# Kernel tuning notes

Measured on AMD Instinct MI355X. Metric: run time of the kernel, lower is better.

The kernel has to match this reference:

```python
import jax, jax.numpy as jnp
import numpy as np

B, T, D = 8192, 12, 512


def setup_inputs() -> dict:
    key = jax.random.key(0)
    ks = jax.random.split(key, 14)
    s = 1.0 / np.sqrt(D)
    return {
        "memory": jax.random.normal(ks[0], (B, D), jnp.float32),
        "info": jax.random.normal(ks[1], (B, D), jnp.float32),
        "control": jax.random.normal(ks[2], (B, D), jnp.float32),
        "contControl": jax.random.normal(ks[3], (B, D), jnp.float32),
        "allControls": jax.random.normal(ks[4], (B, T, D), jnp.float32),
        "allMemories": jax.random.normal(ks[5], (B, T, D), jnp.float32),
        # params (torch nn.Linear convention: W is [out, in])
        "Wc": jax.random.uniform(ks[6], (D, D), jnp.float32, -s, s),
        "bc": jax.random.uniform(ks[7], (D,), jnp.float32, -s, s),
        "Wa": jax.random.uniform(ks[8], (1, D), jnp.float32, -s, s),
        "ba": jax.random.uniform(ks[9], (1,), jnp.float32, -s, s),
        "Wl": jax.random.uniform(ks[10], (D, 3 * D), jnp.float32, -s, s),
        "bl": jax.random.uniform(ks[11], (D,), jnp.float32, -s, s),
        "Wg": jax.random.uniform(ks[12], (D, D), jnp.float32, -s, s),
        "bg": jax.random.uniform(ks[13], (D,), jnp.float32, -s, s),
    }


def reference(memory, info, control, contControl, allControls, allMemories,
              Wc, bc, Wa, ba, Wl, bl, Wg, bg):
    # self-attention over past memories (writeSelfAttMod == 'CONT')
    selfControl = contControl @ Wc.T + bc                      # [B, D]
    interactions = allControls * selfControl[:, None, :]       # [B, T, D]
    attn_logits = jnp.einsum("btd,od->bto", interactions, Wa)[..., 0] + ba[0]  # [B, T]
    attn = jax.nn.softmax(attn_logits, axis=1)                 # [B, T]
    selfSmry = jnp.einsum("bt,btd->bd", attn, allMemories)     # [B, D]
    # gated linear write
    newMemory = jnp.concatenate([memory, info, selfSmry], axis=-1) @ Wl.T + bl  # [B, D]
    z = jax.nn.sigmoid(control @ Wg.T + bg)                    # [B, D]
    return newMemory * z + memory * (1.0 - z)
```

## Files before the change

### kernel.cpp

```cpp
#include <hip/hip_runtime.h>
#include <stdint.h>
#include <math.h>


#define NB 8192
#define NT 12
#define ND 512

typedef short  bf16x8 __attribute__((ext_vector_type(8)));
typedef float  f32x4  __attribute__((ext_vector_type(4)));

__device__ __forceinline__ unsigned short f2bf(float x) {
    uint32_t u = __float_as_uint(x);
    uint32_t r = u + 0x7FFFu + ((u >> 16) & 1u);
    return (unsigned short)(r >> 16);
}
__device__ __forceinline__ float bf2f(unsigned short h) {
    return __uint_as_float(((uint32_t)h) << 16);
}

__global__ __launch_bounds__(256)
void wconv_kernel(const float* __restrict__ W, short* __restrict__ H,
                  short* __restrict__ L, int n4)
{
    int i = blockIdx.x * blockDim.x + threadIdx.x;
    if (i >= n4) return;
    float4 v = reinterpret_cast<const float4*>(W)[i];
    float xs[4] = {v.x, v.y, v.z, v.w};
    short4 hv, lv;
    short hh[4], ll[4];
#pragma unroll
    for (int j = 0; j < 4; ++j) {
        unsigned short h = f2bf(xs[j]);
        unsigned short l = f2bf(xs[j] - bf2f(h));
        hh[j] = (short)h; ll[j] = (short)l;
    }
    hv.x = hh[0]; hv.y = hh[1]; hv.z = hh[2]; hv.w = hh[3];
    lv.x = ll[0]; lv.y = ll[1]; lv.z = ll[2]; lv.w = ll[3];
    reinterpret_cast<short4*>(H)[i] = hv;
    reinterpret_cast<short4*>(L)[i] = lv;
}


template<bool AF32>
__device__ __forceinline__ void run_seg(
    const float* __restrict__ Af,
    const short* __restrict__ Aph, const short* __restrict__ Apl,
    const short* __restrict__ Wph, const short* __restrict__ Wpl,
    int sW,
    short* __restrict__ AhT, short* __restrict__ AlT,
    short* __restrict__ WhT, short* __restrict__ WlT,
    f32x4 (&acc)[4][2],
    const int soff, const int sr, const int sk,
    const int abase, const int wbase)
{
    float4 fa0, fa1;
    bf16x8 pah, pal, pwh, pwl;

    auto do_load = [&](int kt) {
        const int k = kt * 32 + sk;
        if constexpr (AF32) {
            fa0 = *reinterpret_cast<const float4*>(Af + (size_t)sr * ND + k);
            fa1 = *reinterpret_cast<const float4*>(Af + (size_t)sr * ND + k + 4);
        } else {
            pah = *reinterpret_cast<const bf16x8*>(Aph + (size_t)sr * ND + k);
            pal = *reinterpret_cast<const bf16x8*>(Apl + (size_t)sr * ND + k);
        }
        pwh = *reinterpret_cast<const bf16x8*>(Wph + (size_t)sr * sW + k);
        pwl = *reinterpret_cast<const bf16x8*>(Wpl + (size_t)sr * sW + k);
    };
    auto do_write = [&](int buf) {
        const int o = buf * 4096 + soff;
        if constexpr (AF32) {
            float xs[8] = {fa0.x, fa0.y, fa0.z, fa0.w, fa1.x, fa1.y, fa1.z, fa1.w};
            bf16x8 hv, lv;
#pragma unroll
            for (int j = 0; j < 8; ++j) {
                unsigned short h = f2bf(xs[j]);
                unsigned short l = f2bf(xs[j] - bf2f(h));
                hv[j] = (short)h; lv[j] = (short)l;
            }
            *reinterpret_cast<bf16x8*>(AhT + o) = hv;
            *reinterpret_cast<bf16x8*>(AlT + o) = lv;
        } else {
            *reinterpret_cast<bf16x8*>(AhT + o) = pah;
            *reinterpret_cast<bf16x8*>(AlT + o) = pal;
        }
        *reinterpret_cast<bf16x8*>(WhT + o) = pwh;
        *reinterpret_cast<bf16x8*>(WlT + o) = pwl;
    };

    do_load(0);
    do_write(0);
    __syncthreads();
    int cur = 0;
    for (int kt = 0; kt < 16; ++kt) {
        const bool pf = (kt + 1 < 16);
        if (pf) do_load(kt + 1);
        const int cb = cur * 4096;
        bf16x8 ah[4], al[4], wh[2], wl[2];
#pragma unroll
        for (int i = 0; i < 4; ++i) {
            ah[i] = *reinterpret_cast<const bf16x8*>(AhT + cb + abase + i * 512);
            al[i] = *reinterpret_cast<const bf16x8*>(AlT + cb + abase + i * 512);
        }
#pragma unroll
        for (int j = 0; j < 2; ++j) {
            wh[j] = *reinterpret_cast<const bf16x8*>(WhT + cb + wbase + j * 512);
            wl[j] = *reinterpret_cast<const bf16x8*>(WlT + cb + wbase + j * 512);
        }
#pragma unroll
        for (int i = 0; i < 4; ++i)
#pragma unroll
            for (int j = 0; j < 2; ++j) {
                acc[i][j] = __builtin_amdgcn_mfma_f32_16x16x32_bf16(ah[i], wh[j], acc[i][j], 0, 0, 0);
                acc[i][j] = __builtin_amdgcn_mfma_f32_16x16x32_bf16(ah[i], wl[j], acc[i][j], 0, 0, 0);
                acc[i][j] = __builtin_amdgcn_mfma_f32_16x16x32_bf16(al[i], wh[j], acc[i][j], 0, 0, 0);
            }
        if (pf) do_write(cur ^ 1);
        __syncthreads();
        cur ^= 1;
    }
}

#define GEMM_SETUP                                                         \
    const int t = threadIdx.x;                                             \
    const int bm = blockIdx.x, bn = blockIdx.y;                            \
    const int sr = t >> 2, scn = t & 3, sk = scn * 8;                      \
    const int soff = sr * 32 + (scn ^ ((sr >> 1) & 3)) * 8;                \
    const int w = t >> 6, wr = w >> 2, wc = w & 3;                         \
    const int lane = t & 63, fr = lane & 15, q = lane >> 4;                \
    const int rq = (q ^ ((fr >> 1) & 3)) * 8;                              \
    const int abase = (wr * 64 + fr) * 32 + rq;                            \
    const int wbase = (wc * 32 + fr) * 32 + rq;

__global__ __launch_bounds__(512, 2)
void gemm_selfcontrol(const float* __restrict__ cc,
                      const short* __restrict__ wch, const short* __restrict__ wcl,
                      const float* __restrict__ bc,
                      float* __restrict__ sc_out)
{
    __shared__ __align__(16) short AhT[2 * 4096], AlT[2 * 4096];
    __shared__ __align__(16) short WhT[2 * 4096], WlT[2 * 4096];
    GEMM_SETUP
    f32x4 acc[4][2];
    const f32x4 zz = {0.f, 0.f, 0.f, 0.f};
#pragma unroll
    for (int i = 0; i < 4; ++i) { acc[i][0] = zz; acc[i][1] = zz; }

    run_seg<true>(cc + (size_t)bm * 128 * ND, nullptr, nullptr,
                  wch + (size_t)(bn * 128) * ND, wcl + (size_t)(bn * 128) * ND, ND,
                  AhT, AlT, WhT, WlT, acc, soff, sr, sk, abase, wbase);

    const int c0 = bn * 128 + wc * 32 + fr;
    const float bc0 = bc[c0], bc1 = bc[c0 + 16];
#pragma unroll
    for (int i = 0; i < 4; ++i) {
        const int r = bm * 128 + wr * 64 + i * 16 + q * 4;
#pragma unroll
        for (int ri = 0; ri < 4; ++ri) {
            sc_out[(size_t)(r + ri) * ND + c0]      = acc[i][0][ri] + bc0;
            sc_out[(size_t)(r + ri) * ND + c0 + 16] = acc[i][1][ri] + bc1;
        }
    }
}

__global__ __launch_bounds__(512, 2)
void gemm_write(const float* __restrict__ memory, const float* __restrict__ info,
                const float* __restrict__ ctrl,
                const short* __restrict__ sh, const short* __restrict__ sl,
                const short* __restrict__ wlh, const short* __restrict__ wll,
                const short* __restrict__ wgh, const short* __restrict__ wgl,
                const float* __restrict__ bl_, const float* __restrict__ bg_,
                float* __restrict__ out)
{
    __shared__ __align__(16) short AhT[2 * 4096], AlT[2 * 4096];
    __shared__ __align__(16) short WhT[2 * 4096], WlT[2 * 4096];
    GEMM_SETUP
    f32x4 accN[4][2], accZ[4][2];
    const f32x4 zz = {0.f, 0.f, 0.f, 0.f};
#pragma unroll
    for (int i = 0; i < 4; ++i) {
        accN[i][0] = zz; accN[i][1] = zz;
        accZ[i][0] = zz; accZ[i][1] = zz;
    }

    const size_t ar = (size_t)bm * 128 * ND;
    const short* wlh_b = wlh + (size_t)(bn * 128) * 1536;
    const short* wll_b = wll + (size_t)(bn * 128) * 1536;

    run_seg<true >(memory + ar, nullptr, nullptr, wlh_b,        wll_b,        1536,
                   AhT, AlT, WhT, WlT, accN, soff, sr, sk, abase, wbase);
    run_seg<true >(info + ar,   nullptr, nullptr, wlh_b + 512,  wll_b + 512,  1536,
                   AhT, AlT, WhT, WlT, accN, soff, sr, sk, abase, wbase);
    run_seg<false>(nullptr, sh + ar, sl + ar,     wlh_b + 1024, wll_b + 1024, 1536,
                   AhT, AlT, WhT, WlT, accN, soff, sr, sk, abase, wbase);
    run_seg<true >(ctrl + ar,   nullptr, nullptr,
                   wgh + (size_t)(bn * 128) * ND, wgl + (size_t)(bn * 128) * ND, ND,
                   AhT, AlT, WhT, WlT, accZ, soff, sr, sk, abase, wbase);

    const int c0 = bn * 128 + wc * 32 + fr;
    const float blv[2] = {bl_[c0], bl_[c0 + 16]};
    const float bgv[2] = {bg_[c0], bg_[c0 + 16]};
#pragma unroll
    for (int i = 0; i < 4; ++i) {
        const int r = bm * 128 + wr * 64 + i * 16 + q * 4;
#pragma unroll
        for (int ri = 0; ri < 4; ++ri) {
#pragma unroll
            for (int j = 0; j < 2; ++j) {
                const int col = c0 + j * 16;
                const size_t idx = (size_t)(r + ri) * ND + col;
                const float nm = accN[i][j][ri] + blv[j];
                const float zl = accZ[i][j][ri] + bgv[j];
                const float z  = 1.f / (1.f + expf(-zl));
                const float m  = memory[idx];
                out[idx] = (nm - m) * z + m;
            }
        }
    }
}

__global__ __launch_bounds__(256)
void attn_kernel(const float* __restrict__ allControls,
                 const float* __restrict__ allMemories,
                 const float* __restrict__ selfControl,
                 const float* __restrict__ Wa,
                 const float* __restrict__ ba,
                 short* __restrict__ sh, short* __restrict__ sl)
{
    __shared__ float red[4][NT];
    __shared__ float lg[NT];
    const int b = blockIdx.x;
    const int t = threadIdx.x;
    const int lane = t & 63, wv = t >> 6;

    const float2 sc = ((const float2*)(selfControl + (size_t)b * ND))[t];
    const float2 wa = ((const float2*)Wa)[t];
    const float swx = sc.x * wa.x, swy = sc.y * wa.y;

    const float2* ac2 = (const float2*)(allControls + (size_t)b * NT * ND);
    float part[NT];
#pragma unroll
    for (int tt = 0; tt < NT; ++tt) {
        float2 v = ac2[tt * 256 + t];
        part[tt] = fmaf(v.x, swx, v.y * swy);
    }
#pragma unroll
    for (int tt = 0; tt < NT; ++tt) {
        float v = part[tt];
#pragma unroll
        for (int m = 1; m < 64; m <<= 1) v += __shfl_xor(v, m, 64);
        if (lane == 0) red[wv][tt] = v;
    }
    __syncthreads();
    if (t < NT) lg[t] = red[0][t] + red[1][t] + red[2][t] + red[3][t] + ba[0];
    __syncthreads();

    float l[NT], mx = -1e30f;
#pragma unroll
    for (int tt = 0; tt < NT; ++tt) { l[tt] = lg[tt]; mx = fmaxf(mx, l[tt]); }
    float e[NT], s = 0.f;
#pragma unroll
    for (int tt = 0; tt < NT; ++tt) { e[tt] = expf(l[tt] - mx); s += e[tt]; }
    const float inv = 1.f / s;

    const float2* am2 = (const float2*)(allMemories + (size_t)b * NT * ND);
    float ax = 0.f, ay = 0.f;
#pragma unroll
    for (int tt = 0; tt < NT; ++tt) {
        float2 v = am2[tt * 256 + t];
        const float wgt = e[tt] * inv;
        ax = fmaf(wgt, v.x, ax);
        ay = fmaf(wgt, v.y, ay);
    }
    unsigned short hx = f2bf(ax); unsigned short lx = f2bf(ax - bf2f(hx));
    unsigned short hy = f2bf(ay); unsigned short ly = f2bf(ay - bf2f(hy));
    short2 hv; hv.x = (short)hx; hv.y = (short)hy;
    short2 lv; lv.x = (short)lx; lv.y = (short)ly;
    reinterpret_cast<short2*>(sh + (size_t)b * ND)[t] = hv;
    reinterpret_cast<short2*>(sl + (size_t)b * ND)[t] = lv;
}

extern "C" void kernel_launch(void* const* d_in, const int* in_sizes, int n_in,
                              void* d_out, int out_size, void* d_ws, size_t ws_size,
                              hipStream_t stream) {
    const float* memory      = (const float*)d_in[0];
    const float* info        = (const float*)d_in[1];
    const float* control     = (const float*)d_in[2];
    const float* contControl = (const float*)d_in[3];
    const float* allControls = (const float*)d_in[4];
    const float* allMemories = (const float*)d_in[5];
    const float* Wc          = (const float*)d_in[6];
    const float* bc          = (const float*)d_in[7];
    const float* Wl          = (const float*)d_in[10];
    const float* bl          = (const float*)d_in[11];
    const float* Wg          = (const float*)d_in[12];
    const float* bg          = (const float*)d_in[13];
    float* out = (float*)d_out;

    char* wsb = (char*)d_ws;
    float* selfControl = (float*)wsb;
    short* sh  = (short*)(wsb + (size_t)16 * 1024 * 1024);
    short* sl  = sh  + (size_t)NB * ND;
    short* wch = sl  + (size_t)NB * ND;
    short* wcl = wch + 512 * 512;
    short* wlh = wcl + 512 * 512;
    short* wll = wlh + 512 * 1536;
    short* wgh = wll + 512 * 1536;
    short* wgl = wgh + 512 * 512;

    wconv_kernel<<<(512 * 512 / 4 + 255) / 256, 256, 0, stream>>>(Wc, wch, wcl, 512 * 512 / 4);
    wconv_kernel<<<(512 * 1536 / 4 + 255) / 256, 256, 0, stream>>>(Wl, wlh, wll, 512 * 1536 / 4);
    wconv_kernel<<<(512 * 512 / 4 + 255) / 256, 256, 0, stream>>>(Wg, wgh, wgl, 512 * 512 / 4);

    dim3 ggrid(NB / 128, ND / 128);
    gemm_selfcontrol<<<ggrid, 512, 0, stream>>>(contControl, wch, wcl,
                                                (const float*)d_in[7], selfControl);
    attn_kernel<<<NB, 256, 0, stream>>>(allControls, allMemories, selfControl,
                                        (const float*)d_in[8], (const float*)d_in[9],
                                        sh, sl);
    gemm_write<<<ggrid, 512, 0, stream>>>(memory, info, control, sh, sl,
                                          wlh, wll, wgh, wgl, bl, bg, out);
}
```

Measured before the change: 565.0 us.

## Use one wavefront per batch row in attention and merge weight conversions

The attention kernel now gives each batch row to a single 64-lane wavefront with 8 elements per lane. This removes the shared-memory reduction and both block barriers, and uses 16-byte vector loads and stores. The Wa scaling moves into the selfControl GEMM epilogue, so the attention kernel reads one precomputed vector. The bias ba is dropped because softmax does not change under a constant shift. The three weight-conversion launches are merged into one kernel to cut launch overhead.

```diff
diff --git a/kernel.cpp b/kernel.cpp
--- a/kernel.cpp
+++ b/kernel.cpp
@@ -20,25 +20,31 @@
 }
 
 __global__ __launch_bounds__(256)
-void wconv_kernel(const float* __restrict__ W, short* __restrict__ H,
-                  short* __restrict__ L, int n4)
-{
-    int i = blockIdx.x * blockDim.x + threadIdx.x;
-    if (i >= n4) return;
-    float4 v = reinterpret_cast<const float4*>(W)[i];
+void wconv_all(const float* __restrict__ Wc, const float* __restrict__ Wl,
+               const float* __restrict__ Wg,
+               short* __restrict__ wch, short* __restrict__ wcl,
+               short* __restrict__ wlh, short* __restrict__ wll,
+               short* __restrict__ wgh, short* __restrict__ wgl)
+{
+    int i = blockIdx.x * 256 + threadIdx.x;
+    const float* src; short* H; short* L; int j;
+    if (i < 65536)        { src = Wc; H = wch; L = wcl; j = i; }
+    else if (i < 262144)  { src = Wl; H = wlh; L = wll; j = i - 65536; }
+    else                  { src = Wg; H = wgh; L = wgl; j = i - 262144; }
+    float4 v = reinterpret_cast<const float4*>(src)[j];
     float xs[4] = {v.x, v.y, v.z, v.w};
     short4 hv, lv;
     short hh[4], ll[4];
 #pragma unroll
-    for (int j = 0; j < 4; ++j) {
-        unsigned short h = f2bf(xs[j]);
-        unsigned short l = f2bf(xs[j] - bf2f(h));
-        hh[j] = (short)h; ll[j] = (short)l;
+    for (int k = 0; k < 4; ++k) {
+        unsigned short h = f2bf(xs[k]);
+        unsigned short l = f2bf(xs[k] - bf2f(h));
+        hh[k] = (short)h; ll[k] = (short)l;
     }
     hv.x = hh[0]; hv.y = hh[1]; hv.z = hh[2]; hv.w = hh[3];
     lv.x = ll[0]; lv.y = ll[1]; lv.z = ll[2]; lv.w = ll[3];
-    reinterpret_cast<short4*>(H)[i] = hv;
-    reinterpret_cast<short4*>(L)[i] = lv;
+    reinterpret_cast<short4*>(H)[j] = hv;
+    reinterpret_cast<short4*>(L)[j] = lv;
 }
 
 
@@ -137,8 +143,8 @@
 __global__ __launch_bounds__(512, 2)
 void gemm_selfcontrol(const float* __restrict__ cc,
                       const short* __restrict__ wch, const short* __restrict__ wcl,
-                      const float* __restrict__ bc,
-                      float* __restrict__ sc_out)
+                      const float* __restrict__ bc, const float* __restrict__ Wa,
+                      float* __restrict__ v_out)
 {
     __shared__ __align__(16) short AhT[2 * 4096], AlT[2 * 4096];
     __shared__ __align__(16) short WhT[2 * 4096], WlT[2 * 4096];
@@ -154,13 +160,14 @@
 
     const int c0 = bn * 128 + wc * 32 + fr;
     const float bc0 = bc[c0], bc1 = bc[c0 + 16];
+    const float wa0 = Wa[c0], wa1 = Wa[c0 + 16];
 #pragma unroll
     for (int i = 0; i < 4; ++i) {
         const int r = bm * 128 + wr * 64 + i * 16 + q * 4;
 #pragma unroll
         for (int ri = 0; ri < 4; ++ri) {
-            sc_out[(size_t)(r + ri) * ND + c0]      = acc[i][0][ri] + bc0;
-            sc_out[(size_t)(r + ri) * ND + c0 + 16] = acc[i][1][ri] + bc1;
+            v_out[(size_t)(r + ri) * ND + c0]      = (acc[i][0][ri] + bc0) * wa0;
+            v_out[(size_t)(r + ri) * ND + c0 + 16] = (acc[i][1][ri] + bc1) * wa1;
         }
     }
 }
@@ -222,64 +229,67 @@
 }
 
 __global__ __launch_bounds__(256)
-void attn_kernel(const float* __restrict__ allControls,
-                 const float* __restrict__ allMemories,
-                 const float* __restrict__ selfControl,
-                 const float* __restrict__ Wa,
-                 const float* __restrict__ ba,
-                 short* __restrict__ sh, short* __restrict__ sl)
-{
-    __shared__ float red[4][NT];
-    __shared__ float lg[NT];
-    const int b = blockIdx.x;
-    const int t = threadIdx.x;
-    const int lane = t & 63, wv = t >> 6;
-
-    const float2 sc = ((const float2*)(selfControl + (size_t)b * ND))[t];
-    const float2 wa = ((const float2*)Wa)[t];
-    const float swx = sc.x * wa.x, swy = sc.y * wa.y;
-
-    const float2* ac2 = (const float2*)(allControls + (size_t)b * NT * ND);
+void attn_wave(const float* __restrict__ allControls,
+               const float* __restrict__ allMemories,
+               const float* __restrict__ v,
+               short* __restrict__ sh, short* __restrict__ sl)
+{
+    const int gtid = blockIdx.x * 256 + threadIdx.x;
+    const int b    = gtid >> 6;
+    const int lane = gtid & 63;
+    const int e0   = lane * 8;
+
+    const float4* vp = reinterpret_cast<const float4*>(v + (size_t)b * ND + e0);
+    const float4 v0 = vp[0], v1 = vp[1];
+
+    const float* acb = allControls + (size_t)b * NT * ND + e0;
     float part[NT];
 #pragma unroll
     for (int tt = 0; tt < NT; ++tt) {
-        float2 v = ac2[tt * 256 + t];
-        part[tt] = fmaf(v.x, swx, v.y * swy);
+        const float4 c0 = *reinterpret_cast<const float4*>(acb + tt * ND);
+        const float4 c1 = *reinterpret_cast<const float4*>(acb + tt * ND + 4);
+        float p = c0.x * v0.x;
+        p = fmaf(c0.y, v0.y, p); p = fmaf(c0.z, v0.z, p); p = fmaf(c0.w, v0.w, p);
+        p = fmaf(c1.x, v1.x, p); p = fmaf(c1.y, v1.y, p);
+        p = fmaf(c1.z, v1.z, p); p = fmaf(c1.w, v1.w, p);
+        part[tt] = p;
     }
 #pragma unroll
     for (int tt = 0; tt < NT; ++tt) {
-        float v = part[tt];
-#pragma unroll
-        for (int m = 1; m < 64; m <<= 1) v += __shfl_xor(v, m, 64);
-        if (lane == 0) red[wv][tt] = v;
-    }
-    __syncthreads();
-    if (t < NT) lg[t] = red[0][t] + red[1][t] + red[2][t] + red[3][t] + ba[0];
-    __syncthreads();
-
-    float l[NT], mx = -1e30f;
-#pragma unroll
-    for (int tt = 0; tt < NT; ++tt) { l[tt] = lg[tt]; mx = fmaxf(mx, l[tt]); }
+        float p = part[tt];
+#pragma unroll
+        for (int m = 1; m < 64; m <<= 1) p += __shfl_xor(p, m);
+        part[tt] = p;
+    }
+    float mx = part[0];
+#pragma unroll
+    for (int tt = 1; tt < NT; ++tt) mx = fmaxf(mx, part[tt]);
     float e[NT], s = 0.f;
 #pragma unroll
-    for (int tt = 0; tt < NT; ++tt) { e[tt] = expf(l[tt] - mx); s += e[tt]; }
+    for (int tt = 0; tt < NT; ++tt) { e[tt] = expf(part[tt] - mx); s += e[tt]; }
     const float inv = 1.f / s;
 
-    const float2* am2 = (const float2*)(allMemories + (size_t)b * NT * ND);
-    float ax = 0.f, ay = 0.f;
+    const float* amb = allMemories + (size_t)b * NT * ND + e0;
+    float o[8] = {0.f, 0.f, 0.f, 0.f, 0.f, 0.f, 0.f, 0.f};
 #pragma unroll
     for (int tt = 0; tt < NT; ++tt) {
-        float2 v = am2[tt * 256 + t];
-        const float wgt = e[tt] * inv;
-        ax = fmaf(wgt, v.x, ax);
-        ay = fmaf(wgt, v.y, ay);
-    }
-    unsigned short hx = f2bf(ax); unsigned short lx = f2bf(ax - bf2f(hx));
-    unsigned short hy = f2bf(ay); unsigned short ly = f2bf(ay - bf2f(hy));
-    short2 hv; hv.x = (short)hx; hv.y = (short)hy;
-    short2 lv; lv.x = (short)lx; lv.y = (short)ly;
-    reinterpret_cast<short2*>(sh + (size_t)b * ND)[t] = hv;
-    reinterpret_cast<short2*>(sl + (size_t)b * ND)[t] = lv;
+        const float w = e[tt] * inv;
+        const float4 m0 = *reinterpret_cast<const float4*>(amb + tt * ND);
+        const float4 m1 = *reinterpret_cast<const float4*>(amb + tt * ND + 4);
+        o[0] = fmaf(w, m0.x, o[0]); o[1] = fmaf(w, m0.y, o[1]);
+        o[2] = fmaf(w, m0.z, o[2]); o[3] = fmaf(w, m0.w, o[3]);
+        o[4] = fmaf(w, m1.x, o[4]); o[5] = fmaf(w, m1.y, o[5]);
+        o[6] = fmaf(w, m1.z, o[6]); o[7] = fmaf(w, m1.w, o[7]);
+    }
+    bf16x8 hv, lv;
+#pragma unroll
+    for (int j = 0; j < 8; ++j) {
+        unsigned short h = f2bf(o[j]);
+        unsigned short l = f2bf(o[j] - bf2f(h));
+        hv[j] = (short)h; lv[j] = (short)l;
+    }
+    *reinterpret_cast<bf16x8*>(sh + (size_t)b * ND + e0) = hv;
+    *reinterpret_cast<bf16x8*>(sl + (size_t)b * ND + e0) = lv;
 }
 
 extern "C" void kernel_launch(void* const* d_in, const int* in_sizes, int n_in,
@@ -293,6 +303,7 @@
     const float* allMemories = (const float*)d_in[5];
     const float* Wc          = (const float*)d_in[6];
     const float* bc          = (const float*)d_in[7];
+    const float* Wa          = (const float*)d_in[8];
     const float* Wl          = (const float*)d_in[10];
     const float* bl          = (const float*)d_in[11];
     const float* Wg          = (const float*)d_in[12];
@@ -300,7 +311,7 @@
     float* out = (float*)d_out;
 
     char* wsb = (char*)d_ws;
-    float* selfControl = (float*)wsb;
+    float* v   = (float*)wsb;
     short* sh  = (short*)(wsb + (size_t)16 * 1024 * 1024);
     short* sl  = sh  + (size_t)NB * ND;
     short* wch = sl  + (size_t)NB * ND;
@@ -310,16 +321,11 @@
     short* wgh = wll + 512 * 1536;
     short* wgl = wgh + 512 * 512;
 
-    wconv_kernel<<<(512 * 512 / 4 + 255) / 256, 256, 0, stream>>>(Wc, wch, wcl, 512 * 512 / 4);
-    wconv_kernel<<<(512 * 1536 / 4 + 255) / 256, 256, 0, stream>>>(Wl, wlh, wll, 512 * 1536 / 4);
-    wconv_kernel<<<(512 * 512 / 4 + 255) / 256, 256, 0, stream>>>(Wg, wgh, wgl, 512 * 512 / 4);
+    wconv_all<<<1280, 256, 0, stream>>>(Wc, Wl, Wg, wch, wcl, wlh, wll, wgh, wgl);
 
     dim3 ggrid(NB / 128, ND / 128);
-    gemm_selfcontrol<<<ggrid, 512, 0, stream>>>(contControl, wch, wcl,
-                                                (const float*)d_in[7], selfControl);
-    attn_kernel<<<NB, 256, 0, stream>>>(allControls, allMemories, selfControl,
-                                        (const float*)d_in[8], (const float*)d_in[9],
-                                        sh, sl);
+    gemm_selfcontrol<<<ggrid, 512, 0, stream>>>(contControl, wch, wcl, bc, Wa, v);
+    attn_wave<<<NB * 64 / 256, 256, 0, stream>>>(allControls, allMemories, v, sh, sl);
     gemm_write<<<ggrid, 512, 0, stream>>>(memory, info, control, sh, sl,
                                           wlh, wll, wgh, wgl, bl, bg, out);
 }
```

After: 562.6 us. Within noise of the previous version (-0.4%).
